# Optimization experiments

Measured on AMD Instinct MI355X. Metric: run time of the kernel, lower is better.

Reference implementation:

```python
import jax, jax.numpy as jnp
import numpy as np

RUNS = 500; WAYS = 5; SHOT = 5; QUERIES = 15; DIM = 640
NS = WAYS * SHOT; QS = WAYS * QUERIES; N = NS + QS
LAM = 10.0; ALPHA = 0.7; LINK_RATE = 6; UPDATE_RATE = 0.6
K_HOP = 4; EPOCHS = 10; BALANCE = True; SINK_EPS = 1e-3; MAXITERS = 1000
FEAT_SCALE = 0.02  # keeps exp(-lam*d^2) numerically alive (see notes)


def _sqdist(a, b):
    # torch.cdist(a, b).pow(2) == squared euclidean distance, clamped >= 0
    d = (jnp.sum(a * a, -1)[:, :, None] + jnp.sum(b * b, -1)[:, None, :]
         - 2.0 * jnp.einsum('bnd,bmd->bnm', a, b))
    return jnp.maximum(d, 0.0)


def _keep_top_k_row(m, k):
    # zero out all but the k largest entries of each row (torch topk+scatter)
    B, Nn, _ = m.shape
    vals, idx = jax.lax.top_k(m, k)              # [B, Nn, k]
    bi = jnp.arange(B)[:, None, None]
    ri = jnp.arange(Nn)[None, :, None]
    return jnp.zeros_like(m).at[bi, ri, idx].set(vals)


def _graph_convolution(X, A, k):
    Nn = X.shape[1]
    I = jnp.eye(Nn, dtype=X.dtype)[None]
    A = _keep_top_k_row(A, k)
    D = A.sum(-1) ** -0.5
    W = D[:, None, :] * A * D[:, :, None]        # sym-normalized adjacency
    L = 0.5 * I + 0.5 * W
    G = L @ L                                    # matrix_power(L, 2)
    return G @ X, G


def _build_graph(W):
    Nn = W.shape[1]
    I = jnp.eye(Nn, dtype=W.dtype)[None]
    W = W * (1.0 - I)                            # remove self loops
    D = W.sum(-1) ** -0.5
    return D[:, None, :] * W * D[:, :, None]


def _sinkhorn(M, n_l, labels, eps, balance):
    # compute_optimal_transport: data-dependent while loop, on-device cond
    n_runs, n, ways = M.shape
    r = jnp.ones((n_runs, n), M.dtype)
    c = jnp.full((n_runs, ways), float(n // ways), M.dtype)
    onehot = jax.nn.one_hot(labels[:, :n_l], ways, dtype=M.dtype) if n_l > 0 else None

    def cond(state):
        P, u, it = state
        return jnp.logical_and(jnp.max(jnp.abs(u - P.sum(2))) > eps, it <= MAXITERS)

    def body(state):
        P, _, it = state
        u = P.sum(2)
        P = P * (r / u)[:, :, None]
        if balance:
            P = P * (c / P.sum(1))[:, None, :]
        if n_l > 0:
            P = P.at[:, :n_l].set(onehot)        # clamp labeled rows to one-hot
        return P, u, it + 1

    u0 = jnp.zeros((n_runs, n), M.dtype)
    P, _, _ = jax.lax.while_loop(cond, body, (M, u0, jnp.int32(1)))
    return P


def _get_prob(features, proto, ys):
    dist = _sqdist(features, proto)              # [B, N, ways]
    Pq = jnp.exp(-LAM * dist[:, NS:])
    Pq = _sinkhorn(Pq, 0, ys, SINK_EPS, BALANCE)
    Ps = jax.nn.one_hot(ys, WAYS, dtype=features.dtype)
    return jnp.concatenate([Ps, Pq], axis=1)


def _forward(xs, xq, ys, yq):
    features = jnp.concatenate([xs, xq], axis=1)     # [B, N, D]
    labels = jnp.concatenate([ys, yq], axis=1)       # [B, N]
    W = None
    for _ in range(K_HOP):
        dist = jnp.exp(-LAM * _sqdist(features, features))
        features, W = _graph_convolution(features, dist, LINK_RATE)
        W = _build_graph(W)
    proto = features[:, :NS].reshape(features.shape[0], WAYS, SHOT, -1).mean(axis=2)
    W = _build_graph(W)                              # (called twice, as in torch)
    I = jnp.eye(N, dtype=features.dtype)[None]
    Inv = jnp.linalg.inv(I - ALPHA * W)
    for _ in range(EPOCHS):
        Z = _get_prob(features, proto, ys)
        Z = Inv @ Z
        Z = _sinkhorn(Z, NS, ys, SINK_EPS, BALANCE)
        new_proto = jnp.einsum('bnw,bnd->bwd', Z, features) / Z.sum(axis=1)[:, :, None]
        proto = (1.0 - UPDATE_RATE) * proto + UPDATE_RATE * new_proto
    Z = _get_prob(features, proto, ys)
    olabels = jnp.argmax(Z, axis=2)
    matches = (labels == olabels).astype(jnp.float32)
    return matches[:, NS:].mean(axis=1)              # per-episode query accuracy [B]


def setup_inputs() -> dict:
    key = jax.random.key(0)
    k1, k2, k3, k4 = jax.random.split(key, 4)
    xs = jax.random.normal(k1, (RUNS, NS, DIM), jnp.float32) * FEAT_SCALE
    xq = jax.random.normal(k2, (RUNS, QS, DIM), jnp.float32) * FEAT_SCALE
    ys = jax.random.randint(k3, (RUNS, NS), 0, WAYS)
    yq = jax.random.randint(k4, (RUNS, QS), 0, WAYS)
    return {"xs": xs, "xq": xq, "ys": ys, "yq": yq}


def reference(xs, xq, ys, yq):
    return _forward(xs, xq, ys, yq)
```

## Files before the change

kernel.cpp:

```cpp
#include <hip/hip_runtime.h>

#define B_RUNS 500
#define WAYS   5
#define NSUP   25
#define NQ     75
#define NN     100
#define DIM    640
#define TOPK   6
#define KHOP   4
#define NEPOCH 10

#define CTRL_BYTES 262144
#define KB2    250
#define NBK    25
#define BPB    10
#define NROUND 512
#define READYB 0x80000000u

#define EP_FLT   20224
#define GF_OFF   0
#define INV_OFF  10000

#define GS   101
#define DYN_LDS_BYTES (NN * GS * 4)

#if defined(__has_builtin)
#if __has_builtin(__builtin_amdgcn_permlane32_swap)
#define HAVE_PLSWAP 1
#endif
#endif

template <int CTRL>
__device__ __forceinline__ float dpp_addf(float v) {
  int r = __builtin_amdgcn_update_dpp(0, __float_as_int(v), CTRL, 0xF, 0xF, false);
  return v + __int_as_float(r);
}
template <int PAT>
__device__ __forceinline__ float swz_addf(float v) {
  return v + __int_as_float(__builtin_amdgcn_ds_swizzle(__float_as_int(v), PAT));
}
__device__ __forceinline__ float swap32_addf(float v) {
#ifdef HAVE_PLSWAP
  int x = __float_as_int(v);
  auto r = __builtin_amdgcn_permlane32_swap(x, x, false, false);
  return __int_as_float(r[0]) + __int_as_float(r[1]);
#else
  return v + __shfl_xor(v, 32, 64);
#endif
}
__device__ __forceinline__ float wsum64f_fast(float v) {
  v = dpp_addf<0x121>(v);
  v = dpp_addf<0x122>(v);
  v = dpp_addf<0x124>(v);
  v = dpp_addf<0x128>(v);
  v = swz_addf<0x401F>(v);
  v = swap32_addf(v);
  return __int_as_float(__builtin_amdgcn_readfirstlane(__float_as_int(v)));
}
__device__ __forceinline__ float frcpf(float x) {
#if __has_builtin(__builtin_amdgcn_rcpf)
  float r = __builtin_amdgcn_rcpf(x);
#else
  float r = 1.0f / x;
#endif
  float e = fmaf(-x, r, 1.0f);
  r = fmaf(r, e, r);
  return r;
}

__device__ unsigned grid_barrier_max(unsigned* ctrlu, int b, unsigned rnd, unsigned lm) {
  unsigned r = rnd < (NROUND - 1) ? rnd : (NROUND - 1);
  const int bk = b % NBK;
  unsigned* barr  = ctrlu + bk * NROUND + r;
  unsigned* bmax  = ctrlu + (NBK + bk) * NROUND + r;
  unsigned* marr  = ctrlu + 2 * NBK * NROUND + r;
  unsigned* mmax  = ctrlu + 2 * NBK * NROUND + NROUND + r;
  unsigned* bflag = ctrlu + (2 * NBK + 2) * NROUND + bk * NROUND + r;

  __hip_atomic_fetch_max(bmax, lm, __ATOMIC_RELAXED, __HIP_MEMORY_SCOPE_AGENT);
  unsigned a = __hip_atomic_fetch_add(barr, 1u, __ATOMIC_ACQ_REL, __HIP_MEMORY_SCOPE_AGENT);
  long sp = 0;
  if (a == (unsigned)(BPB - 1)) {
    unsigned bm = __hip_atomic_load(bmax, __ATOMIC_RELAXED, __HIP_MEMORY_SCOPE_AGENT);
    __hip_atomic_fetch_max(mmax, bm, __ATOMIC_RELAXED, __HIP_MEMORY_SCOPE_AGENT);
    __hip_atomic_fetch_add(marr, 1u, __ATOMIC_ACQ_REL, __HIP_MEMORY_SCOPE_AGENT);
    while (__hip_atomic_load(marr, __ATOMIC_RELAXED, __HIP_MEMORY_SCOPE_AGENT) < (unsigned)NBK) {
      __builtin_amdgcn_s_sleep(2);
      if (++sp > 50000000L) break;
    }
    __builtin_amdgcn_fence(__ATOMIC_ACQUIRE, "agent");
    unsigned g = __hip_atomic_load(mmax, __ATOMIC_RELAXED, __HIP_MEMORY_SCOPE_AGENT);
    __hip_atomic_store(bflag, g | READYB, __ATOMIC_RELEASE, __HIP_MEMORY_SCOPE_AGENT);
    return g;
  } else {
    unsigned f;
    while (!((f = __hip_atomic_load(bflag, __ATOMIC_RELAXED, __HIP_MEMORY_SCOPE_AGENT)) & READYB)) {
      __builtin_amdgcn_s_sleep(4);
      if (++sp > 50000000L) break;
    }
    __builtin_amdgcn_fence(__ATOMIC_ACQUIRE, "agent");
    return f & ~READYB;
  }
}

__global__ __launch_bounds__(512, 6) void k1_lds(const float* __restrict__ xs,
                                                 const float* __restrict__ xq,
                                                 char* __restrict__ wsb) {
  extern __shared__ float dynf[];
  float* G   = dynf;
  float* STf = dynf;

  const int b = blockIdx.x;
  float* GfF  = (float*)(wsb + CTRL_BYTES) + (size_t)b * EP_FLT;
  float* InvF = GfF + INV_OFF;

  __shared__ float nsh[NN], Dsh[NN], rowk[NN], colk[NN];
  __shared__ float wS[NN][7];
  __shared__ int   idxS[NN][7];
  __shared__ int   cntS[NN];

  const int t  = threadIdx.x;

  {
    const int tx = t & 31;
    const int ty = t >> 5;
    int ia[7], ja[4];
    #pragma unroll
    for (int a = 0; a < 7; ++a) { int v = ty + 16 * a; ia[a] = v < NN ? v : NN - 1; }
    #pragma unroll
    for (int c = 0; c < 4; ++c) { int v = tx + 32 * c; ja[c] = v < NN ? v : NN - 1; }

    float acc[7][4];
    #pragma unroll
    for (int a = 0; a < 7; ++a)
      #pragma unroll
      for (int c = 0; c < 4; ++c) acc[a][c] = 0.0f;
    const float* xsb = xs + (size_t)b * NSUP * DIM;
    const float* xqb = xq + (size_t)b * NQ * DIM;
    for (int chunk = 0; chunk < 40; ++chunk) {
      int k0 = chunk * 16;
      for (int e = t; e < NN * 16; e += 512) {
        int r = e >> 4, km = e & 15;
        int k = k0 + km;
        float v = (r < NSUP) ? xsb[r * DIM + k] : xqb[(r - NSUP) * DIM + k];
        STf[(km >> 1) * 202 + 2 * r + (km & 1)] = v;
      }
      __syncthreads();
      #pragma unroll 2
      for (int m = 0; m < 8; ++m) {
        float2 rv[7], cv[4];
        #pragma unroll
        for (int a = 0; a < 7; ++a) rv[a] = *(const float2*)(STf + m * 202 + 2 * ia[a]);
        #pragma unroll
        for (int c = 0; c < 4; ++c) cv[c] = *(const float2*)(STf + m * 202 + 2 * ja[c]);
        #pragma unroll
        for (int a = 0; a < 7; ++a)
          #pragma unroll
          for (int c = 0; c < 4; ++c) {
            acc[a][c] = fmaf(rv[a].x, cv[c].x, acc[a][c]);
            acc[a][c] = fmaf(rv[a].y, cv[c].y, acc[a][c]);
          }
      }
      __syncthreads();
    }
    #pragma unroll
    for (int a = 0; a < 7; ++a)
      #pragma unroll
      for (int c = 0; c < 4; ++c) {
        int i = ty + 16 * a, j = tx + 32 * c;
        if (i < NN && j < NN) G[i * GS + j] = acc[a][c];
      }
    __syncthreads();
  }

  for (int hop = 0; hop < KHOP; ++hop) {
    if (t < NN) nsh[t] = G[t * GS + t];
    __syncthreads();
    int kj[TOPK]; float ke[TOPK];
    if (t < NN) {
      unsigned long long m0 = 0ull, m1 = 0ull;
      const float nt = nsh[t];
      for (int s = 0; s < TOPK; ++s) {
        float best = 3.0e38f; int bj = 0;
        for (int j = 0; j < NN; ++j) {
          unsigned long long bit = (j < 64) ? ((m0 >> j) & 1ull) : ((m1 >> (j - 64)) & 1ull);
          if (bit) continue;
          float d = (nt + nsh[j]) - 2.0f * G[t * GS + j];
          d = d > 0.0f ? d : 0.0f;
          if (d < best) { best = d; bj = j; }
        }
        if (bj < 64) m0 |= 1ull << bj; else m1 |= 1ull << (bj - 64);
      }
      float s = 0.0f;
      unsigned long long mm0 = m0, mm1 = m1;
      #pragma unroll
      for (int sidx = 0; sidx < TOPK; ++sidx) {
        int j;
        if (mm0) { j = __ffsll((long long)mm0) - 1; mm0 &= mm0 - 1; }
        else     { j = 64 + __ffsll((long long)mm1) - 1; mm1 &= mm1 - 1; }
        float d = (nt + nsh[j]) - 2.0f * G[t * GS + j];
        d = d > 0.0f ? d : 0.0f;
        float e = expf(-10.0f * d);
        kj[sidx] = j; ke[sidx] = e;
        s += e;
      }
      Dsh[t] = 1.0f / sqrtf(s);
    }
    __syncthreads();
    if (t < NN) {
      int cnt = 0; bool sd = false;
      float dt = Dsh[t];
      #pragma unroll
      for (int sidx = 0; sidx < TOPK; ++sidx) {
        int j = kj[sidx];
        float lw = 0.5f * ((Dsh[j] * ke[sidx]) * dt);
        if (j == t) { lw = 0.5f + lw; sd = true; }
        else if (!sd && j > t) { idxS[t][cnt] = t; wS[t][cnt] = 0.5f; ++cnt; sd = true; }
        idxS[t][cnt] = j; wS[t][cnt] = lw; ++cnt;
      }
      if (!sd) { idxS[t][cnt] = t; wS[t][cnt] = 0.5f; ++cnt; }
      cntS[t] = cnt;
    }
    __syncthreads();

    {
      const int wv8 = t >> 6, ln = t & 63;
      const int i2 = ln + 64;
      const bool h2 = (i2 < NN);
      const int r1 = h2 ? i2 : 0;
      float lw0[7], lw1[7]; int li0[7], li1[7];
      {
        int c0 = cntS[ln];
        int c1 = h2 ? cntS[r1] : 0;
        #pragma unroll
        for (int s2 = 0; s2 < 7; ++s2) {
          lw0[s2] = (s2 < c0) ? wS[ln][s2] : 0.0f;
          li0[s2] = (s2 < c0) ? idxS[ln][s2] : 0;
          lw1[s2] = (s2 < c1) ? wS[r1][s2] : 0.0f;
          li1[s2] = (s2 < c1) ? idxS[r1][s2] : 0;
        }
      }
      #pragma unroll 1
      for (int pair = 0; pair < 2; ++pair) {
        for (int c = wv8; c < NN; c += 8) {
          float o0 = 0.0f, o1 = 0.0f;
          #pragma unroll
          for (int s2 = 0; s2 < 7; ++s2) o0 = fmaf(lw0[s2], G[li0[s2] * GS + c], o0);
          #pragma unroll
          for (int s2 = 0; s2 < 7; ++s2) o1 = fmaf(lw1[s2], G[li1[s2] * GS + c], o1);
          asm volatile("s_waitcnt lgkmcnt(0)" ::: "memory");
          G[ln * GS + c] = o0;
          if (h2) G[i2 * GS + c] = o1;
        }
        __syncthreads();
        for (int r = wv8; r < NN; r += 8) {
          float o0 = 0.0f, o1 = 0.0f;
          #pragma unroll
          for (int s2 = 0; s2 < 7; ++s2) o0 = fmaf(lw0[s2], G[r * GS + li0[s2]], o0);
          #pragma unroll
          for (int s2 = 0; s2 < 7; ++s2) o1 = fmaf(lw1[s2], G[r * GS + li1[s2]], o1);
          asm volatile("s_waitcnt lgkmcnt(0)" ::: "memory");
          G[r * GS + ln] = o0;
          if (h2) G[r * GS + i2] = o1;
        }
        __syncthreads();
      }
    }

    if (hop == KHOP - 1) {
      for (int e = t; e < NN * NN; e += 512) GfF[e] = G[(e / NN) * GS + (e % NN)];
      __syncthreads();
      if (t < NN) {
        for (int j = 0; j < NN; ++j) G[t * GS + j] = 0.0f;
        int cnt = cntS[t];
        for (int s2 = 0; s2 < cnt; ++s2) {
          float w1 = wS[t][s2]; int k = idxS[t][s2];
          int c2 = cntS[k];
          for (int t2 = 0; t2 < c2; ++t2)
            G[t * GS + idxS[k][t2]] += w1 * wS[k][t2];
        }
      }
      __syncthreads();
      for (int rep = 0; rep < 2; ++rep) {
        if (t < NN) G[t * GS + t] = 0.0f;
        __syncthreads();
        if (t < NN) {
          float s = 0.0f;
          for (int j = 0; j < NN; ++j) s += G[t * GS + j];
          Dsh[t] = 1.0f / sqrtf(s);
        }
        __syncthreads();
        for (int e = t; e < NN * NN; e += 512) {
          int i = e / NN, j = e % NN;
          G[i * GS + j] = (Dsh[j] * G[i * GS + j]) * Dsh[i];
        }
        __syncthreads();
      }
      for (int e = t; e < NN * NN; e += 512) {
        int i = e / NN, j = e % NN;
        G[i * GS + j] = ((i == j) ? 1.0f : 0.0f) - 0.7f * G[i * GS + j];
      }
      __syncthreads();
      for (int k = 0; k < NN; ++k) {
        if (t < NN) { rowk[t] = G[k * GS + t]; colk[t] = G[t * GS + k]; }
        __syncthreads();
        float pinv = 1.0f / rowk[k];
        for (int e = t; e < NN * NN; e += 512) {
          int i = e / NN, j = e % NN;
          float v;
          if (i == k)      v = (j == k) ? pinv : rowk[j] * pinv;
          else if (j == k) v = -(colk[i] * pinv);
          else             v = G[i * GS + j] - colk[i] * (rowk[j] * pinv);
          G[i * GS + j] = v;
        }
        __syncthreads();
      }
      for (int e = t; e < NN * NN; e += 512) InvF[e] = G[(e / NN) * GS + (e % NN)];
    }
  }
}

__global__ __launch_bounds__(512) void k2_epochs(const int* __restrict__ ys,
                                                 const int* __restrict__ yq,
                                                 char* __restrict__ wsb,
                                                 float* __restrict__ out) {
  const int blk = blockIdx.x;
  const int t   = threadIdx.x;
  const int epw = t >> 8;
  const int tl  = t & 255;
  const int wvl = (t >> 6) & 3;
  const int ln  = t & 63;
  const int b   = blk * 2 + epw;
  const float* Gq   = (const float*)(wsb + CTRL_BYTES) + (size_t)b * EP_FLT;
  const float* Invq = Gq + INV_OFF;
  unsigned* ctrlu = (unsigned*)wsb;

  __shared__ float Z[2][NN * WAYS];
  __shared__ float gvF[2][WAYS * NN];
  __shared__ float pbuf[2][4][WAYS * NN];
  __shared__ float betaS[2][WAYS][NN];
  __shared__ float nrmS[2][NN];
  __shared__ float csv[2][WAYS], pnS[2][WAYS];
  __shared__ int ysS[2][NSUP];
  __shared__ unsigned mS[2];
  __shared__ unsigned Tsh;
  __shared__ int redi[2];

  unsigned rnd = 0;

  if (tl < NSUP) ysS[epw][tl] = ys[b * NSUP + tl];
  if (tl < NN)   nrmS[epw][tl] = Gq[tl * NN + tl];
  for (int e = tl; e < WAYS * NN; e += 256) {
    int w = e / NN, n = e % NN;
    betaS[epw][w][n] = (n >= w * 5 && n < w * 5 + 5) ? 0.2f : 0.0f;
  }
  __syncthreads();

  auto sinkhorn = [&](int base, int n, float cval, bool clamp) {
    const bool own = (wvl == 0);
    const int r0 = ln, r1 = ln + 64;
    const bool h1 = (r1 < n);
    float p0[WAYS], p1[WAYS];
    float up0 = 0.f, up1 = 0.f, u0 = 0.f, u1 = 0.f;
    int aflag = 0;
    int m = 0; int ysq = -1;
    if (own) {
      #pragma unroll
      for (int w = 0; w < WAYS; ++w) {
        p0[w] = Z[epw][(base + r0) * WAYS + w];
        p1[w] = h1 ? Z[epw][(base + r1) * WAYS + w] : 0.f;
      }
      if (clamp && r0 < NSUP) ysq = ysS[epw][r0];
      u0 = p0[0] + p0[1] + p0[2] + p0[3] + p0[4];
      if (h1) u1 = p1[0] + p1[1] + p1[2] + p1[3] + p1[4];
      float dl = fabsf(up0 - u0);
      if (h1) dl = fmaxf(dl, fabsf(up1 - u1));
      aflag = __any(dl > 1e-3f);
    }
    unsigned target = 0;
    for (;;) {
      if (own) {
        while (m < 1000 && ((unsigned)m < target || aflag)) {
          float i0 = frcpf(u0);
          #pragma unroll
          for (int w = 0; w < WAYS; ++w) p0[w] *= i0;
          up0 = u0;
          if (h1) {
            float i1 = frcpf(u1);
            #pragma unroll
            for (int w = 0; w < WAYS; ++w) p1[w] *= i1;
            up1 = u1;
          }
          #pragma unroll
          for (int w = 0; w < WAYS; ++w) {
            float s = wsum64f_fast(p0[w] + (h1 ? p1[w] : 0.f));
            float f = cval * frcpf(s);
            p0[w] *= f;
            if (h1) p1[w] *= f;
          }
          if (clamp && r0 < NSUP) {
            #pragma unroll
            for (int w = 0; w < WAYS; ++w) p0[w] = (ysq == w) ? 1.f : 0.f;
          }
          ++m;
          u0 = p0[0] + p0[1] + p0[2] + p0[3] + p0[4];
          if (h1) u1 = p1[0] + p1[1] + p1[2] + p1[3] + p1[4];
          if ((unsigned)m >= target) {
            float dl = fabsf(up0 - u0);
            if (h1) dl = fmaxf(dl, fabsf(up1 - u1));
            aflag = __any(dl > 1e-3f);
          } else {
            aflag = 1;
          }
        }
        if (ln == 0) mS[epw] = (unsigned)m;
      }
      __syncthreads();
      if (t == 0) {
        unsigned lm = mS[0] > mS[1] ? mS[0] : mS[1];
        Tsh = grid_barrier_max(ctrlu, blk, rnd, lm);
      }
      __syncthreads();
      ++rnd;
      unsigned T = Tsh;
      if (T == target) break;
      target = T;
    }
    if (own) {
      #pragma unroll
      for (int w = 0; w < WAYS; ++w) {
        Z[epw][(base + r0) * WAYS + w] = p0[w];
        if (h1) Z[epw][(base + r1) * WAYS + w] = p1[w];
      }
    }
    __syncthreads();
  };

  for (int epi = 0; epi <= NEPOCH; ++epi) {
    {
      float a0[WAYS], a1[WAYS];
      #pragma unroll
      for (int w = 0; w < WAYS; ++w) { a0[w] = 0.f; a1[w] = 0.f; }
      int k0 = wvl * 25;
      for (int kk = 0; kk < 25; ++kk) {
        int k = k0 + kk;
        float g0 = Gq[(size_t)k * NN + ln];
        float g1 = (ln < NN - 64) ? Gq[(size_t)k * NN + 64 + ln] : 0.f;
        #pragma unroll
        for (int w = 0; w < WAYS; ++w) {
          float bw = betaS[epw][w][k];
          a0[w] = fmaf(g0, bw, a0[w]);
          a1[w] = fmaf(g1, bw, a1[w]);
        }
      }
      #pragma unroll
      for (int w = 0; w < WAYS; ++w) {
        pbuf[epw][wvl][w * NN + ln] = a0[w];
        if (ln < NN - 64) pbuf[epw][wvl][w * NN + 64 + ln] = a1[w];
      }
    }
    __syncthreads();
    for (int e = tl; e < WAYS * NN; e += 256)
      gvF[epw][e] = ((pbuf[epw][0][e] + pbuf[epw][1][e]) + pbuf[epw][2][e]) + pbuf[epw][3][e];
    __syncthreads();
    if (tl < WAYS) {
      float s = 0.f;
      for (int n = 0; n < NN; ++n) s = fmaf(betaS[epw][tl][n], gvF[epw][tl * NN + n], s);
      pnS[epw][tl] = s;
    }
    __syncthreads();
    for (int e = tl; e < NQ * WAYS; e += 256) {
      int r = NSUP + e / WAYS, w = e % WAYS;
      float d = (nrmS[epw][r] + pnS[epw][w]) - 2.0f * gvF[epw][w * NN + r];
      Z[epw][r * WAYS + w] = expf(-10.0f * (d > 0.f ? d : 0.f));
    }
    __syncthreads();
    sinkhorn(NSUP, NQ, 15.0f, false);

    if (epi == NEPOCH) {
      if (tl == 0) redi[epw] = 0;
      __syncthreads();
      if (tl < NQ) {
        int row = NSUP + tl;
        float bv = Z[epw][row * WAYS + 0]; int am = 0;
        #pragma unroll
        for (int w = 1; w < WAYS; ++w) {
          float v = Z[epw][row * WAYS + w];
          if (v > bv) { bv = v; am = w; }
        }
        if (am == yq[b * NQ + tl]) atomicAdd(&redi[epw], 1);
      }
      __syncthreads();
      if (tl == 0) out[b] = (float)redi[epw] / 75.0f;
    } else {
      if (tl < NSUP) {
        #pragma unroll
        for (int w = 0; w < WAYS; ++w) Z[epw][tl * WAYS + w] = (ysS[epw][tl] == w) ? 1.f : 0.f;
      }
      __syncthreads();
      for (int r = wvl; r < NN; r += 4) {
        float a0 = 0, a1 = 0, a2 = 0, a3 = 0, a4 = 0;
        for (int k = ln; k < NN; k += 64) {
          float iv = Invq[(size_t)r * NN + k];
          a0 = fmaf(iv, Z[epw][k * WAYS + 0], a0);
          a1 = fmaf(iv, Z[epw][k * WAYS + 1], a1);
          a2 = fmaf(iv, Z[epw][k * WAYS + 2], a2);
          a3 = fmaf(iv, Z[epw][k * WAYS + 3], a3);
          a4 = fmaf(iv, Z[epw][k * WAYS + 4], a4);
        }
        a0 = wsum64f_fast(a0); a1 = wsum64f_fast(a1); a2 = wsum64f_fast(a2);
        a3 = wsum64f_fast(a3); a4 = wsum64f_fast(a4);
        if (ln == 0) {
          pbuf[epw][0][r * WAYS + 0] = a0; pbuf[epw][0][r * WAYS + 1] = a1;
          pbuf[epw][0][r * WAYS + 2] = a2; pbuf[epw][0][r * WAYS + 3] = a3;
          pbuf[epw][0][r * WAYS + 4] = a4;
        }
      }
      __syncthreads();
      for (int e = tl; e < NN * WAYS; e += 256) Z[epw][e] = pbuf[epw][0][e];
      __syncthreads();
      sinkhorn(0, NN, 20.0f, true);
      if (tl < WAYS) {
        float s = 0.f;
        for (int r = 0; r < NN; ++r) s += Z[epw][r * WAYS + tl];
        csv[epw][tl] = s;
      }
      __syncthreads();
      for (int e = tl; e < NN * WAYS; e += 256) {
        int n = e / WAYS, w = e % WAYS;
        float nb = Z[epw][n * WAYS + w] / csv[epw][w];
        betaS[epw][w][n] = 0.4f * betaS[epw][w][n] + 0.6f * nb;
      }
      __syncthreads();
    }
  }
}

extern "C" void kernel_launch(void* const* d_in, const int* in_sizes, int n_in,
                              void* d_out, int out_size, void* d_ws, size_t ws_size,
                              hipStream_t stream) {
  const float* xs = (const float*)d_in[0];
  const float* xq = (const float*)d_in[1];
  const int*   ys = (const int*)d_in[2];
  const int*   yq = (const int*)d_in[3];
  float* out = (float*)d_out;
  char* ws   = (char*)d_ws;

  hipMemsetAsync(d_ws, 0, CTRL_BYTES, stream);

  (void)hipFuncSetAttribute((const void*)k1_lds,
                            hipFuncAttributeMaxDynamicSharedMemorySize,
                            DYN_LDS_BYTES);
  hipLaunchKernelGGL(k1_lds, dim3(B_RUNS), dim3(512), DYN_LDS_BYTES, stream, xs, xq, ws);
  hipLaunchKernelGGL(k2_epochs, dim3(KB2), dim3(512), 0, stream, ys, yq, ws, out);
}
```

Baseline: 1.585 ms.

## Double-buffer pivot row/col in Gauss-Jordan inverse, vectorize Gram staging loads

The Gauss-Jordan inversion now keeps pivot row and column in double-buffered shared arrays. Each elimination step writes the next pivot's row and column as it goes, so one barrier per pivot is removed along with the separate load phase, and the per-element div/mod indexing is replaced by incremental index stepping. The Gram-matrix staging loop now uses float4 global loads with a float4 LDS layout, which halves the LDS read count per FMA. It also changes which wave owns the sinkhorn rows in the epochs kernel, which spreads that work across waves for the two episodes. Each inner loop pass now carries a little extra conditional logic.

```diff
diff --git a/kernel.cpp b/kernel.cpp
--- a/kernel.cpp
+++ b/kernel.cpp
@@ -114,7 +114,8 @@
   float* GfF  = (float*)(wsb + CTRL_BYTES) + (size_t)b * EP_FLT;
   float* InvF = GfF + INV_OFF;
 
-  __shared__ float nsh[NN], Dsh[NN], rowk[NN], colk[NN];
+  __shared__ float nsh[NN], Dsh[NN];
+  __shared__ float rowkA[NN], colkA[NN], rowkB[NN], colkB[NN];
   __shared__ float wS[NN][7];
   __shared__ int   idxS[NN][7];
   __shared__ int   cntS[NN];
@@ -139,26 +140,29 @@
     const float* xqb = xq + (size_t)b * NQ * DIM;
     for (int chunk = 0; chunk < 40; ++chunk) {
       int k0 = chunk * 16;
-      for (int e = t; e < NN * 16; e += 512) {
-        int r = e >> 4, km = e & 15;
-        int k = k0 + km;
-        float v = (r < NSUP) ? xsb[r * DIM + k] : xqb[(r - NSUP) * DIM + k];
-        STf[(km >> 1) * 202 + 2 * r + (km & 1)] = v;
-      }
-      __syncthreads();
-      #pragma unroll 2
-      for (int m = 0; m < 8; ++m) {
-        float2 rv[7], cv[4];
-        #pragma unroll
-        for (int a = 0; a < 7; ++a) rv[a] = *(const float2*)(STf + m * 202 + 2 * ia[a]);
-        #pragma unroll
-        for (int c = 0; c < 4; ++c) cv[c] = *(const float2*)(STf + m * 202 + 2 * ja[c]);
+      if (t < 400) {
+        int r = t >> 2, kq = t & 3;
+        const float* src = (r < NSUP) ? (xsb + r * DIM + k0 + 4 * kq)
+                                      : (xqb + (r - NSUP) * DIM + k0 + 4 * kq);
+        float4 v = *(const float4*)src;
+        *(float4*)(STf + kq * 404 + 4 * r) = v;
+      }
+      __syncthreads();
+      #pragma unroll 1
+      for (int q = 0; q < 4; ++q) {
+        float4 rv[7], cv[4];
+        #pragma unroll
+        for (int a = 0; a < 7; ++a) rv[a] = *(const float4*)(STf + q * 404 + 4 * ia[a]);
+        #pragma unroll
+        for (int c = 0; c < 4; ++c) cv[c] = *(const float4*)(STf + q * 404 + 4 * ja[c]);
         #pragma unroll
         for (int a = 0; a < 7; ++a)
           #pragma unroll
           for (int c = 0; c < 4; ++c) {
             acc[a][c] = fmaf(rv[a].x, cv[c].x, acc[a][c]);
             acc[a][c] = fmaf(rv[a].y, cv[c].y, acc[a][c]);
+            acc[a][c] = fmaf(rv[a].z, cv[c].z, acc[a][c]);
+            acc[a][c] = fmaf(rv[a].w, cv[c].w, acc[a][c]);
           }
       }
       __syncthreads();
@@ -301,19 +305,33 @@
         G[i * GS + j] = ((i == j) ? 1.0f : 0.0f) - 0.7f * G[i * GS + j];
       }
       __syncthreads();
-      for (int k = 0; k < NN; ++k) {
-        if (t < NN) { rowk[t] = G[k * GS + t]; colk[t] = G[t * GS + k]; }
-        __syncthreads();
-        float pinv = 1.0f / rowk[k];
-        for (int e = t; e < NN * NN; e += 512) {
-          int i = e / NN, j = e % NN;
-          float v;
-          if (i == k)      v = (j == k) ? pinv : rowk[j] * pinv;
-          else if (j == k) v = -(colk[i] * pinv);
-          else             v = G[i * GS + j] - colk[i] * (rowk[j] * pinv);
-          G[i * GS + j] = v;
-        }
-        __syncthreads();
+      if (t < NN) { rowkA[t] = G[t]; colkA[t] = G[t * GS]; }
+      __syncthreads();
+      {
+        float* rC = rowkA; float* cC = colkA;
+        float* rN = rowkB; float* cN = colkB;
+        const int i0 = t / NN, j0 = t - i0 * NN;
+        const int a0 = i0 * GS + j0;
+        for (int k = 0; k < NN; ++k) {
+          float pinv = 1.0f / rC[k];
+          int i = i0, j = j0, addr = a0;
+          for (int e = t; e < NN * NN; e += 512) {
+            float rj = rC[j], ci = cC[i];
+            float v;
+            if (i == k)      v = (j == k) ? pinv : rj * pinv;
+            else if (j == k) v = -(ci * pinv);
+            else             v = G[addr] - ci * (rj * pinv);
+            G[addr] = v;
+            if (i == k + 1) rN[j] = v;
+            if (j == k + 1) cN[i] = v;
+            i += 5; j += 12; addr += 5 * GS + 12;
+            if (j >= NN) { j -= NN; i += 1; addr += GS - NN; }
+          }
+          __syncthreads();
+          float* tp;
+          tp = rC; rC = rN; rN = tp;
+          tp = cC; cC = cN; cN = tp;
+        }
       }
       for (int e = t; e < NN * NN; e += 512) InvF[e] = G[(e / NN) * GS + (e % NN)];
     }
@@ -357,7 +375,7 @@
   __syncthreads();
 
   auto sinkhorn = [&](int base, int n, float cval, bool clamp) {
-    const bool own = (wvl == 0);
+    const bool own = (wvl == epw);
     const int r0 = ln, r1 = ln + 64;
     const bool h1 = (r1 < n);
     float p0[WAYS], p1[WAYS];
```

Measured after the change: 1.668 ms. 5.2% more time.

## Retile Gram prologue to exact 5x4 per thread with double-buffered float4 staging

Applied to the files above, without the earlier changes.

The 100x100 feature Gram computation now maps 500 threads onto an exact 20x25 grid with 5x4 outputs each, removing the clamped duplicate rows and columns of the old 7x4 mapping. Staging moves to float4 loads into two LDS buffers. The next chunk is prefetched into registers while the current one is computed, so each chunk needs one barrier instead of two. The Sinkhorn owner-wave test also changes from wave 0 to the wave matching the episode slot, which shifts which wave does that work.

```diff
diff --git a/kernel.cpp b/kernel.cpp
--- a/kernel.cpp
+++ b/kernel.cpp
@@ -122,54 +122,72 @@
   const int t  = threadIdx.x;
 
   {
-    const int tx = t & 31;
-    const int ty = t >> 5;
-    int ia[7], ja[4];
+    const int tx = t % 25;
+    const int ty = t / 25;
+    const bool act = (t < 500);
+    const int tyc = act ? ty : 19;
+    int ia[5], ja[4];
     #pragma unroll
-    for (int a = 0; a < 7; ++a) { int v = ty + 16 * a; ia[a] = v < NN ? v : NN - 1; }
+    for (int a = 0; a < 5; ++a) ia[a] = tyc + 20 * a;
     #pragma unroll
-    for (int c = 0; c < 4; ++c) { int v = tx + 32 * c; ja[c] = v < NN ? v : NN - 1; }
-
-    float acc[7][4];
+    for (int c = 0; c < 4; ++c) ja[c] = tx + 25 * c;
+
+    float acc[5][4];
     #pragma unroll
-    for (int a = 0; a < 7; ++a)
+    for (int a = 0; a < 5; ++a)
       #pragma unroll
       for (int c = 0; c < 4; ++c) acc[a][c] = 0.0f;
+
     const float* xsb = xs + (size_t)b * NSUP * DIM;
     const float* xqb = xq + (size_t)b * NQ * DIM;
+    float* B0 = STf;
+    float* B1 = STf + 1616;
+    const int r_  = t >> 2;
+    const int kq_ = t & 3;
+    const bool stg = (t < 400);
+    const float* srcb = stg ? ((r_ < NSUP) ? (xsb + r_ * DIM)
+                                           : (xqb + (r_ - NSUP) * DIM)) : xsb;
+    if (stg) {
+      float4 v = *(const float4*)(srcb + 4 * kq_);
+      *(float4*)(B0 + kq_ * 404 + 4 * r_) = v;
+    }
+    __syncthreads();
+
+    #pragma unroll 1
     for (int chunk = 0; chunk < 40; ++chunk) {
-      int k0 = chunk * 16;
-      for (int e = t; e < NN * 16; e += 512) {
-        int r = e >> 4, km = e & 15;
-        int k = k0 + km;
-        float v = (r < NSUP) ? xsb[r * DIM + k] : xqb[(r - NSUP) * DIM + k];
-        STf[(km >> 1) * 202 + 2 * r + (km & 1)] = v;
-      }
-      __syncthreads();
-      #pragma unroll 2
-      for (int m = 0; m < 8; ++m) {
-        float2 rv[7], cv[4];
-        #pragma unroll
-        for (int a = 0; a < 7; ++a) rv[a] = *(const float2*)(STf + m * 202 + 2 * ia[a]);
-        #pragma unroll
-        for (int c = 0; c < 4; ++c) cv[c] = *(const float2*)(STf + m * 202 + 2 * ja[c]);
-        #pragma unroll
-        for (int a = 0; a < 7; ++a)
+      float* cur = (chunk & 1) ? B1 : B0;
+      float* nxt = (chunk & 1) ? B0 : B1;
+      float4 v;
+      const bool more = stg && (chunk + 1 < 40);
+      if (more) v = *(const float4*)(srcb + (chunk + 1) * 16 + 4 * kq_);
+      #pragma unroll 1
+      for (int q = 0; q < 4; ++q) {
+        const float* cq = cur + q * 404;
+        float4 cv[4];
+        #pragma unroll
+        for (int c = 0; c < 4; ++c) cv[c] = *(const float4*)(cq + 4 * ja[c]);
+        #pragma unroll
+        for (int a = 0; a < 5; ++a) {
+          float4 rv = *(const float4*)(cq + 4 * ia[a]);
           #pragma unroll
           for (int c = 0; c < 4; ++c) {
-            acc[a][c] = fmaf(rv[a].x, cv[c].x, acc[a][c]);
-            acc[a][c] = fmaf(rv[a].y, cv[c].y, acc[a][c]);
+            acc[a][c] = fmaf(rv.x, cv[c].x, acc[a][c]);
+            acc[a][c] = fmaf(rv.y, cv[c].y, acc[a][c]);
+            acc[a][c] = fmaf(rv.z, cv[c].z, acc[a][c]);
+            acc[a][c] = fmaf(rv.w, cv[c].w, acc[a][c]);
           }
-      }
-      __syncthreads();
-    }
-    #pragma unroll
-    for (int a = 0; a < 7; ++a)
-      #pragma unroll
-      for (int c = 0; c < 4; ++c) {
-        int i = ty + 16 * a, j = tx + 32 * c;
-        if (i < NN && j < NN) G[i * GS + j] = acc[a][c];
-      }
+        }
+      }
+      if (more) *(float4*)(nxt + kq_ * 404 + 4 * r_) = v;
+      __syncthreads();
+    }
+    if (act) {
+      #pragma unroll
+      for (int a = 0; a < 5; ++a)
+        #pragma unroll
+        for (int c = 0; c < 4; ++c)
+          G[ia[a] * GS + ja[c]] = acc[a][c];
+    }
     __syncthreads();
   }
 
@@ -357,7 +375,7 @@
   __syncthreads();
 
   auto sinkhorn = [&](int base, int n, float cval, bool clamp) {
-    const bool own = (wvl == 0);
+    const bool own = (wvl == epw);
     const int r0 = ln, r1 = ln + 64;
     const bool h1 = (r1 < n);
     float p0[WAYS], p1[WAYS];
```

New measurement: 1.528 ms. 3.6% less time.
